# Kernel tuning notes

Hardware: AMD Instinct MI355X
Metric: run time of the kernel (lower is better)

## Reference

```python
import jax, jax.numpy as jnp
import numpy as np

N = 2048
H = W = 128


def setup_inputs() -> dict:
    key = jax.random.key(0)
    ks = jax.random.split(key, 8)
    # Gaussians placed in front of a pinhole camera at the origin (+z forward)
    xy = jax.random.normal(ks[0], (N, 2), dtype=jnp.float32) * 1.5
    z = jax.random.uniform(ks[1], (N, 1), dtype=jnp.float32, minval=2.0, maxval=6.0)
    mean = jnp.concatenate([xy, z], axis=-1)
    qvec = jax.random.normal(ks[2], (N, 4), dtype=jnp.float32)
    # raw scales -> exp activation gives scales around 0.05
    svec_raw = jax.random.normal(ks[3], (N, 3), dtype=jnp.float32) * 0.3 - 3.0
    color_raw = jax.random.normal(ks[4], (N, 3), dtype=jnp.float32)
    alpha_raw = jax.random.normal(ks[5], (N,), dtype=jnp.float32)
    bg = jax.random.uniform(ks[6], (3,), dtype=jnp.float32)
    viewmat = jnp.eye(4, dtype=jnp.float32)
    intrins = jnp.array([120.0, 120.0, W / 2.0, H / 2.0], dtype=jnp.float32)  # fx fy cx cy
    return dict(mean=mean, qvec=qvec, svec_raw=svec_raw, color_raw=color_raw,
                alpha_raw=alpha_raw, bg=bg, viewmat=viewmat, intrins=intrins)


def _quat_to_rotmat(q):
    q = q / jnp.linalg.norm(q, axis=-1, keepdims=True)
    w, x, y, z = q[..., 0], q[..., 1], q[..., 2], q[..., 3]
    R = jnp.stack([
        1 - 2 * (y * y + z * z), 2 * (x * y - w * z), 2 * (x * z + w * y),
        2 * (x * y + w * z), 1 - 2 * (x * x + z * z), 2 * (y * z - w * x),
        2 * (x * z - w * y), 2 * (y * z + w * x), 1 - 2 * (x * x + y * y),
    ], axis=-1)
    return R.reshape(q.shape[:-1] + (3, 3))


def reference(mean, qvec, svec_raw, color_raw, alpha_raw, bg, viewmat, intrins):
    fx, fy, cx, cy = intrins[0], intrins[1], intrins[2], intrins[3]
    # activations used by GaussianSplattingRenderer (svec_act=exp, alpha/color=sigmoid)
    svec = jnp.exp(svec_raw)
    alpha = jax.nn.sigmoid(alpha_raw)
    color = jax.nn.sigmoid(color_raw)

    Rw = viewmat[:3, :3]
    tw = viewmat[:3, 3]
    p_cam = mean @ Rw.T + tw                      # (N,3)
    x, y, z = p_cam[:, 0], p_cam[:, 1], p_cam[:, 2]
    zc = jnp.maximum(z, 1e-3)

    # 3D covariance Sigma = R diag(s)^2 R^T  via  M = R diag(s),  Sigma = M M^T
    Rq = _quat_to_rotmat(qvec)                    # (N,3,3)
    M = Rq * svec[:, None, :]                     # (N,3,3)

    # perspective Jacobian (EWA splatting), composed with view rotation
    zeros = jnp.zeros_like(zc)
    J = jnp.stack([
        jnp.stack([fx / zc, zeros, -fx * x / (zc * zc)], axis=-1),
        jnp.stack([zeros, fy / zc, -fy * y / (zc * zc)], axis=-1),
    ], axis=-2)                                   # (N,2,3)
    T = jnp.einsum('nij,jk->nik', J, Rw)          # (N,2,3)
    TM = jnp.einsum('nij,njk->nik', T, M)         # (N,2,3)
    cov2d = jnp.einsum('nij,nkj->nik', TM, TM)    # (N,2,2)
    cov2d = cov2d + 0.3 * jnp.eye(2, dtype=cov2d.dtype)  # low-pass filter

    a = cov2d[:, 0, 0]; b = cov2d[:, 0, 1]; c = cov2d[:, 1, 1]
    det = a * c - b * b
    det_safe = jnp.maximum(det, 1e-8)
    conic_a = c / det_safe; conic_b = -b / det_safe; conic_c = a / det_safe

    # projected 2D means
    u = fx * x / zc + cx
    v = fy * y / zc + cy

    px = jnp.arange(W, dtype=jnp.float32) + 0.5
    py = jnp.arange(H, dtype=jnp.float32) + 0.5
    dx = px[:, None] - u[None, :]                 # (W,N)
    dy = py[:, None] - v[None, :]                 # (H,N)

    power = (-0.5 * (conic_a * dx * dx)[None, :, :]
             - 0.5 * (conic_c * dy * dy)[:, None, :]
             - conic_b[None, None, :] * dx[None, :, :] * dy[:, None, :])  # (H,W,N)
    g = jnp.exp(jnp.minimum(power, 0.0))
    valid = (z > 0.2) & (det > 0)
    alpha_pix = jnp.where(valid[None, None, :], jnp.minimum(0.99, alpha * g), 0.0)

    # front-to-back depth order, sequential alpha compositing via cumprod
    order = jnp.argsort(z)
    alpha_s = alpha_pix[:, :, order]              # (H,W,N)
    color_s = color[order]                        # (N,3)
    Tcum = jnp.cumprod(1.0 - alpha_s, axis=-1)
    Tprev = jnp.concatenate([jnp.ones_like(Tcum[..., :1]), Tcum[..., :-1]], axis=-1)
    wgt = alpha_s * Tprev                         # (H,W,N)
    img = jnp.einsum('hwn,nc->hwc', wgt, color_s) + Tcum[..., -1:] * bg
    return img
```

## Files before the change

### kernel.cpp

```cpp
#include <hip/hip_runtime.h>
#include <math.h>

#define NG 2048
#define IMG_W 128
#define IMG_H 128
#define L2E 1.4426950408889634f

typedef unsigned long long u64;

__device__ __forceinline__ float rlf(float x, int i) {
    return __int_as_float(__builtin_amdgcn_readlane(__float_as_int(x), i));
}

struct PrepOut {
    float u, v, A, B, C, al, cr, cg, cb, z, r2;
};

template <bool COLORS>
__device__ __forceinline__ PrepOut prep_g(
    int g,
    const float* __restrict__ mean, const float* __restrict__ qvec,
    const float* __restrict__ svec_raw, const float* __restrict__ color_raw,
    const float* __restrict__ alpha_raw,
    float fx, float fy, float cx, float cy,
    float R00, float R01, float R02, float t0,
    float R10, float R11, float R12, float t1,
    float R20, float R21, float R22, float t2)
{
    PrepOut o;
    float mx = mean[g * 3 + 0], my = mean[g * 3 + 1], mz = mean[g * 3 + 2];
    float x = R00 * mx + R01 * my + R02 * mz + t0;
    float y = R10 * mx + R11 * my + R12 * mz + t1;
    float z = R20 * mx + R21 * my + R22 * mz + t2;
    float zc = fmaxf(z, 0.001f);

    float qw = qvec[g * 4 + 0], qx = qvec[g * 4 + 1];
    float qy = qvec[g * 4 + 2], qz = qvec[g * 4 + 3];
    float qn = rsqrtf(qw * qw + qx * qx + qy * qy + qz * qz);
    qw *= qn; qx *= qn; qy *= qn; qz *= qn;
    float Rq00 = 1.f - 2.f * (qy * qy + qz * qz), Rq01 = 2.f * (qx * qy - qw * qz), Rq02 = 2.f * (qx * qz + qw * qy);
    float Rq10 = 2.f * (qx * qy + qw * qz), Rq11 = 1.f - 2.f * (qx * qx + qz * qz), Rq12 = 2.f * (qy * qz - qw * qx);
    float Rq20 = 2.f * (qx * qz - qw * qy), Rq21 = 2.f * (qy * qz + qw * qx), Rq22 = 1.f - 2.f * (qx * qx + qy * qy);

    float s0 = expf(svec_raw[g * 3 + 0]);
    float s1 = expf(svec_raw[g * 3 + 1]);
    float s2 = expf(svec_raw[g * 3 + 2]);
    float M00 = Rq00 * s0, M01 = Rq01 * s1, M02 = Rq02 * s2;
    float M10 = Rq10 * s0, M11 = Rq11 * s1, M12 = Rq12 * s2;
    float M20 = Rq20 * s0, M21 = Rq21 * s1, M22 = Rq22 * s2;

    float iz = 1.0f / zc;
    float J00 = fx * iz, J02 = -fx * x * iz * iz;
    float J11 = fy * iz, J12 = -fy * y * iz * iz;
    float T00 = J00 * R00 + J02 * R20;
    float T01 = J00 * R01 + J02 * R21;
    float T02 = J00 * R02 + J02 * R22;
    float T10 = J11 * R10 + J12 * R20;
    float T11 = J11 * R11 + J12 * R21;
    float T12 = J11 * R12 + J12 * R22;
    float TM00 = T00 * M00 + T01 * M10 + T02 * M20;
    float TM01 = T00 * M01 + T01 * M11 + T02 * M21;
    float TM02 = T00 * M02 + T01 * M12 + T02 * M22;
    float TM10 = T10 * M00 + T11 * M10 + T12 * M20;
    float TM11 = T10 * M01 + T11 * M11 + T12 * M21;
    float TM12 = T10 * M02 + T11 * M12 + T12 * M22;
    float a = TM00 * TM00 + TM01 * TM01 + TM02 * TM02 + 0.3f;
    float b = TM00 * TM10 + TM01 * TM11 + TM02 * TM12;
    float c = TM10 * TM10 + TM11 * TM11 + TM12 * TM12 + 0.3f;
    float det = a * c - b * b;
    float det_safe = fmaxf(det, 1e-8f);
    float inv_det = 1.0f / det_safe;
    bool valid = (z > 0.2f) && (det > 0.0f);

    float conic_a = c * inv_det;
    float conic_b = -b * inv_det;
    float conic_c = a * inv_det;

    float half_tr = 0.5f * (conic_a + conic_c);
    float half_df = 0.5f * (conic_a - conic_c);
    float lam_min = half_tr - sqrtf(half_df * half_df + conic_b * conic_b);
    float r2 = (lam_min > 1e-20f) ? (1.05f * 2.0f * 24.0f / (L2E * lam_min)) : 3.0e38f;
    if (!valid) r2 = -1.0f;

    o.u = fx * x * iz + cx;
    o.v = fy * y * iz + cy;
    o.A = -0.5f * L2E * conic_a;
    o.B = -L2E * conic_b;
    o.C = -0.5f * L2E * conic_c;
    o.z = z;
    o.r2 = r2;
    if (COLORS) {
        o.al = 1.0f / (1.0f + expf(-alpha_raw[g]));
        o.cr = 1.0f / (1.0f + expf(-color_raw[g * 3 + 0]));
        o.cg = 1.0f / (1.0f + expf(-color_raw[g * 3 + 1]));
        o.cb = 1.0f / (1.0f + expf(-color_raw[g * 3 + 2]));
    } else {
        o.al = o.cr = o.cg = o.cb = 0.f;
    }
    return o;
}

template <int NO>
__device__ __forceinline__ void sort_ranks(const u64* zkey,
                                           unsigned short* ssid,
                                           int K, int t)
{
    u64 myk[NO];
    int myr[NO];
#pragma unroll
    for (int o = 0; o < NO; ++o) {
        int j = t + 256 * o;
        myk[o] = (j < K) ? zkey[j] : ~0ull;
        myr[o] = 0;
    }
    const ulonglong2* z2 = (const ulonglong2*)zkey;
    const int np = (K + 1) >> 1;
    for (int i = 0; i < np; ++i) {
        ulonglong2 kk = z2[i];
#pragma unroll
        for (int o = 0; o < NO; ++o) {
            myr[o] += (kk.x < myk[o]) ? 1 : 0;
            myr[o] += (kk.y < myk[o]) ? 1 : 0;
        }
    }
#pragma unroll
    for (int o = 0; o < NO; ++o) {
        int j = t + 256 * o;
        if (j < K) ssid[myr[o]] = (unsigned short)(myk[o] & 0xFFFFu);
    }
}

__global__ __launch_bounds__(256) void splat_kernel(
    const float* __restrict__ mean, const float* __restrict__ qvec,
    const float* __restrict__ svec_raw, const float* __restrict__ color_raw,
    const float* __restrict__ alpha_raw, const float* __restrict__ bg,
    const float* __restrict__ viewmat, const float* __restrict__ intrins,
    float* __restrict__ out)
{
    __shared__ __align__(16) u64 zkey[NG + 2];
    __shared__ unsigned short ssid[NG];
    __shared__ float4 part[4][64];
    __shared__ int scnt;

    const int t = threadIdx.x;
    const int wave = t >> 6;
    const int lane = t & 63;
    const int tx = blockIdx.x, ty = blockIdx.y;

    if (t == 0) scnt = 0;

    const float fx = intrins[0], fy = intrins[1], cx = intrins[2], cy = intrins[3];
    const float R00 = viewmat[0], R01 = viewmat[1], R02 = viewmat[2],  t0 = viewmat[3];
    const float R10 = viewmat[4], R11 = viewmat[5], R12 = viewmat[6],  t1 = viewmat[7];
    const float R20 = viewmat[8], R21 = viewmat[9], R22 = viewmat[10], t2 = viewmat[11];

    const float x0 = tx * 8 + 0.5f, x1 = x0 + 7.0f;
    const float y0 = ty * 8 + 0.5f, y1 = y0 + 7.0f;

    __syncthreads();

    for (int k = 0; k < 8; ++k) {
        int g = k * 256 + t;
        PrepOut p = prep_g<false>(g, mean, qvec, svec_raw, color_raw,
                                  alpha_raw, fx, fy, cx, cy,
                                  R00, R01, R02, t0, R10, R11, R12, t1,
                                  R20, R21, R22, t2);
        float dxm = fmaxf(0.f, fmaxf(x0 - p.u, p.u - x1));
        float dym = fmaxf(0.f, fmaxf(y0 - p.v, p.v - y1));
        if (dxm * dxm + dym * dym <= p.r2) {
            int slot = atomicAdd(&scnt, 1);
            zkey[slot] = ((u64)__float_as_uint(p.z) << 16) | (unsigned)g;
        }
    }
    __syncthreads();
    const int K = scnt;
    if (t == 0) zkey[K] = ~0ull;
    __syncthreads();

    {
        const int nt = (K + 255) >> 8;
        if (nt <= 1)      sort_ranks<1>(zkey, ssid, K, t);
        else if (nt == 2) sort_ranks<2>(zkey, ssid, K, t);
        else if (nt == 3) sort_ranks<3>(zkey, ssid, K, t);
        else if (nt == 4) sort_ranks<4>(zkey, ssid, K, t);
        else              sort_ranks<8>(zkey, ssid, K, t);
    }
    __syncthreads();

    const float fpx = tx * 8 + (lane & 7) + 0.5f;
    const float fpy = ty * 8 + (lane >> 3) + 0.5f;
    float T = 1.f, Cr = 0.f, Cg = 0.f, Cb = 0.f;

    const int Kq = (K + 3) >> 2;
    const int s0 = wave * Kq;
    const int s1 = min(K, s0 + Kq);

    for (int base = s0; base < s1; base += 64) {
        const int j = base + lane;
        const bool inr = (j < s1);
        const int idx = inr ? (int)ssid[j] : 0;
        PrepOut p = prep_g<true>(idx, mean, qvec, svec_raw, color_raw,
                                 alpha_raw, fx, fy, cx, cy,
                                 R00, R01, R02, t0, R10, R11, R12, t1,
                                 R20, R21, R22, t2);
        u64 mask = __ballot(inr);
        while (mask) {
            const int i = (int)__builtin_ctzll(mask);
            mask &= mask - 1;
            float gu = rlf(p.u, i), gv_ = rlf(p.v, i);
            float gA = rlf(p.A, i), gB = rlf(p.B, i), gC = rlf(p.C, i);
            float al = rlf(p.al, i);
            float cr = rlf(p.cr, i), cg = rlf(p.cg, i), cb = rlf(p.cb, i);

            float dx = fpx - gu;
            float dy = fpy - gv_;
            float adx2 = gA * dx * dx;
            float bdx = gB * dx;
            float pw = fminf(fmaf(dy, fmaf(gC, dy, bdx), adx2), 0.f);
            float gv = exp2f(pw);
            float a = fminf(0.99f, al * gv);
            float w = a * T;
            Cr = fmaf(w, cr, Cr); Cg = fmaf(w, cg, Cg); Cb = fmaf(w, cb, Cb);
            T = fmaf(-a, T, T);
        }
        if (__all(T < 1e-6f)) break;
    }

    part[wave][lane] = make_float4(Cr, Cg, Cb, T);
    __syncthreads();

    if (wave == 0) {
        float4 p0 = part[0][lane];
        float4 p1 = part[1][lane];
        float4 p2 = part[2][lane];
        float4 p3 = part[3][lane];
        float t01 = p0.w * p1.w;
        float t012 = t01 * p2.w;
        float R = p0.x + p0.w * p1.x + t01 * p2.x + t012 * p3.x;
        float G = p0.y + p0.w * p1.y + t01 * p2.y + t012 * p3.y;
        float Bc = p0.z + p0.w * p1.z + t01 * p2.z + t012 * p3.z;
        float Tt = t012 * p3.w;
        const int col = tx * 8 + (lane & 7);
        const int row = ty * 8 + (lane >> 3);
        const int pix = row * IMG_W + col;
        out[pix * 3 + 0] = R + Tt * bg[0];
        out[pix * 3 + 1] = G + Tt * bg[1];
        out[pix * 3 + 2] = Bc + Tt * bg[2];
    }
}

extern "C" void kernel_launch(void* const* d_in, const int* in_sizes, int n_in,
                              void* d_out, int out_size, void* d_ws, size_t ws_size,
                              hipStream_t stream)
{
    const float* mean      = (const float*)d_in[0];
    const float* qvec      = (const float*)d_in[1];
    const float* svec_raw  = (const float*)d_in[2];
    const float* color_raw = (const float*)d_in[3];
    const float* alpha_raw = (const float*)d_in[4];
    const float* bg        = (const float*)d_in[5];
    const float* viewmat   = (const float*)d_in[6];
    const float* intrins   = (const float*)d_in[7];
    float* out = (float*)d_out;
    (void)d_ws; (void)ws_size;

    hipLaunchKernelGGL(splat_kernel, dim3(16, 16), dim3(256), 0, stream,
                       mean, qvec, svec_raw, color_raw, alpha_raw, bg,
                       viewmat, intrins, out);
}
```

Measured before the change: 80.87 us.

## Quadruple block size to 1024 threads and split compositing across 16 waves

Raises the block from 256 to 1024 threads, so culling, rank sorting and per-pixel compositing are spread over 16 waves instead of 4. Each wave composites a contiguous depth slice of the sorted list, and the slices are merged front-to-back with a generic loop. This is meant to cut the serial per-wave compositing chain and the prep/sort work per thread, since only 256 blocks run on a large GPU. In exchange it adds more partials to merge, weakens the early-termination benefit (later waves do work that may be occluded), and 1024-thread blocks may lower register occupancy.

```diff
diff --git a/kernel.cpp b/kernel.cpp
--- a/kernel.cpp
+++ b/kernel.cpp
@@ -5,6 +5,8 @@
 #define IMG_W 128
 #define IMG_H 128
 #define L2E 1.4426950408889634f
+#define BLK 1024
+#define NWAVE 16
 
 typedef unsigned long long u64;
 
@@ -109,7 +111,7 @@
     int myr[NO];
 #pragma unroll
     for (int o = 0; o < NO; ++o) {
-        int j = t + 256 * o;
+        int j = t + BLK * o;
         myk[o] = (j < K) ? zkey[j] : ~0ull;
         myr[o] = 0;
     }
@@ -125,12 +127,12 @@
     }
 #pragma unroll
     for (int o = 0; o < NO; ++o) {
-        int j = t + 256 * o;
+        int j = t + BLK * o;
         if (j < K) ssid[myr[o]] = (unsigned short)(myk[o] & 0xFFFFu);
     }
 }
 
-__global__ __launch_bounds__(256) void splat_kernel(
+__global__ __launch_bounds__(BLK) void splat_kernel(
     const float* __restrict__ mean, const float* __restrict__ qvec,
     const float* __restrict__ svec_raw, const float* __restrict__ color_raw,
     const float* __restrict__ alpha_raw, const float* __restrict__ bg,
@@ -139,7 +141,7 @@
 {
     __shared__ __align__(16) u64 zkey[NG + 2];
     __shared__ unsigned short ssid[NG];
-    __shared__ float4 part[4][64];
+    __shared__ float4 part[NWAVE][64];
     __shared__ int scnt;
 
     const int t = threadIdx.x;
@@ -159,8 +161,9 @@
 
     __syncthreads();
 
-    for (int k = 0; k < 8; ++k) {
-        int g = k * 256 + t;
+#pragma unroll
+    for (int k = 0; k < NG / BLK; ++k) {
+        int g = k * BLK + t;
         PrepOut p = prep_g<false>(g, mean, qvec, svec_raw, color_raw,
                                   alpha_raw, fx, fy, cx, cy,
                                   R00, R01, R02, t0, R10, R11, R12, t1,
@@ -177,21 +180,15 @@
     if (t == 0) zkey[K] = ~0ull;
     __syncthreads();
 
-    {
-        const int nt = (K + 255) >> 8;
-        if (nt <= 1)      sort_ranks<1>(zkey, ssid, K, t);
-        else if (nt == 2) sort_ranks<2>(zkey, ssid, K, t);
-        else if (nt == 3) sort_ranks<3>(zkey, ssid, K, t);
-        else if (nt == 4) sort_ranks<4>(zkey, ssid, K, t);
-        else              sort_ranks<8>(zkey, ssid, K, t);
-    }
+    if (K <= BLK) sort_ranks<1>(zkey, ssid, K, t);
+    else          sort_ranks<2>(zkey, ssid, K, t);
     __syncthreads();
 
     const float fpx = tx * 8 + (lane & 7) + 0.5f;
     const float fpy = ty * 8 + (lane >> 3) + 0.5f;
     float T = 1.f, Cr = 0.f, Cg = 0.f, Cb = 0.f;
 
-    const int Kq = (K + 3) >> 2;
+    const int Kq = (K + NWAVE - 1) / NWAVE;
     const int s0 = wave * Kq;
     const int s1 = min(K, s0 + Kq);
 
@@ -230,22 +227,21 @@
     __syncthreads();
 
     if (wave == 0) {
-        float4 p0 = part[0][lane];
-        float4 p1 = part[1][lane];
-        float4 p2 = part[2][lane];
-        float4 p3 = part[3][lane];
-        float t01 = p0.w * p1.w;
-        float t012 = t01 * p2.w;
-        float R = p0.x + p0.w * p1.x + t01 * p2.x + t012 * p3.x;
-        float G = p0.y + p0.w * p1.y + t01 * p2.y + t012 * p3.y;
-        float Bc = p0.z + p0.w * p1.z + t01 * p2.z + t012 * p3.z;
-        float Tt = t012 * p3.w;
+        float4 acc = part[0][lane];
+#pragma unroll
+        for (int s = 1; s < NWAVE; ++s) {
+            float4 p = part[s][lane];
+            acc.x = fmaf(acc.w, p.x, acc.x);
+            acc.y = fmaf(acc.w, p.y, acc.y);
+            acc.z = fmaf(acc.w, p.z, acc.z);
+            acc.w *= p.w;
+        }
         const int col = tx * 8 + (lane & 7);
         const int row = ty * 8 + (lane >> 3);
         const int pix = row * IMG_W + col;
-        out[pix * 3 + 0] = R + Tt * bg[0];
-        out[pix * 3 + 1] = G + Tt * bg[1];
-        out[pix * 3 + 2] = Bc + Tt * bg[2];
+        out[pix * 3 + 0] = acc.x + acc.w * bg[0];
+        out[pix * 3 + 1] = acc.y + acc.w * bg[1];
+        out[pix * 3 + 2] = acc.z + acc.w * bg[2];
     }
 }
 
@@ -264,7 +260,7 @@
     float* out = (float*)d_out;
     (void)d_ws; (void)ws_size;
 
-    hipLaunchKernelGGL(splat_kernel, dim3(16, 16), dim3(256), 0, stream,
+    hipLaunchKernelGGL(splat_kernel, dim3(16, 16), dim3(BLK), 0, stream,
                        mean, qvec, svec_raw, color_raw, alpha_raw, bg,
                        viewmat, intrins, out);
 }
```

New measurement: 78.67 us. 2.7% less time.
